# Performance work log

Hardware: AMD Instinct MI355X
Metric: run time of the kernel (lower is better)

The kernel has to match this reference:

```python
import jax, jax.numpy as jnp
import numpy as np

EPS = 1e-6
D = 512      # embedding_dim
M = 4        # n_modules
B = 4        # batch
S = 128      # seq_len
K = 32       # stack_size
STEPS = 16   # max_steps (ACT)
SCALE = D ** (-0.5)


def _clin(zr, zi, Wr, Wi, sub):
    # complex linear: (Wr + i Wi)(zr + i zi), torch Linear convention y = x @ W.T
    yr = jnp.einsum(sub, zr, Wr) - jnp.einsum(sub, zi, Wi)
    yi = jnp.einsum(sub, zi, Wr) + jnp.einsum(sub, zr, Wi)
    return yr, yi


def forward_fn(x_real, x_imag, Wl_r, Wl_i, Wq_r, Wq_i, Wk_r, Wk_i, Wv_r, Wv_i,
               ln_scale, ln_shift, mod_bias, gate_mask,
               score_w, score_b, conf_w, conf_b, halt_w, halt_b,
               ctrl_w, ctrl_b, st_score_w, st_score_b, st_conf_w, st_conf_b):
    mem0 = jnp.zeros((B, K, 2 * D), x_real.dtype)
    ptr0 = jnp.zeros((B, K), x_real.dtype).at[:, 0].set(1.0)
    acc0 = jnp.zeros((B, S, 2 * D), x_real.dtype)
    rem0 = jnp.ones((B,), x_real.dtype)

    def step(carry, _):
        sr, si, mem, ptr, acc, rem = carry
        # ComplexAttentionBlock (all M modules vectorized on axis m)
        cr = 0.5 * x_real + 0.5 * sr
        ci = 0.5 * x_imag + 0.5 * si
        zr, zi = _clin(cr, ci, Wl_r, Wl_i, 'bsd,mod->bmso')   # [B,M,S,D]
        # ComplexLayerNorm (magnitude LN, unbiased var as torch.var default)
        mag = jnp.sqrt(zr * zr + zi * zi) + EPS
        mean = mag.mean(-1, keepdims=True)
        var = mag.var(-1, keepdims=True, ddof=1)
        nm = (mag - mean) / jnp.sqrt(var + EPS)
        nm = nm * ln_scale[None, :, None, :] + ln_shift[None, :, None, :]
        ph = jnp.arctan2(zi, zr)
        zr = nm * jnp.cos(ph)
        zi = nm * jnp.sin(ph)
        # ModReLU
        nrm = jnp.sqrt(zr * zr + zi * zi) + EPS
        sc = jax.nn.relu(nrm + mod_bias[None, :, None, :]) / nrm
        zr = zr * sc
        zi = zi * sc
        # ComplexAttention over concatenated real/imag q,k
        sub = 'bmsd,mod->bmso'
        qr, qi = _clin(zr, zi, Wq_r, Wq_i, sub)
        kr, ki = _clin(zr, zi, Wk_r, Wk_i, sub)
        vr, vi = _clin(zr, zi, Wv_r, Wv_i, sub)
        qf = jnp.concatenate([qr, qi], -1)   # [B,M,S,2D]
        kf = jnp.concatenate([kr, ki], -1)
        attn = jax.nn.softmax(jnp.einsum('bmse,bmte->bmst', qf, kf) * SCALE, axis=-1)
        ar = jnp.einsum('bmst,bmtd->bmsd', attn, vr)
        ai = jnp.einsum('bmst,bmtd->bmsd', attn, vi)
        # SigmoidGatingMask
        g = jax.nn.sigmoid(gate_mask)[None, :, None, :]
        pr = ar * g
        pi = ai * g
        flat = jnp.concatenate([pr, pi], -1)  # [B,M,S,2D]
        score = jnp.einsum('bmse,me->bms', flat, score_w) + score_b[None, :, None]
        conf = jax.nn.sigmoid(jnp.einsum('bmse,me->bms', flat, conf_w) + conf_b[None, :, None])
        halt = jnp.einsum('bmse,me->bms', flat, halt_w) + halt_b[None, :, None]
        # DifferentiableStack on seq-pooled broadcast state
        flat_in = jnp.concatenate([sr.mean(1), si.mean(1)], -1)  # [B,2D]
        control = jax.nn.softmax(flat_in @ ctrl_w + ctrl_b, axis=-1)  # [B,3]
        push, pop, noop = control[:, 0:1], control[:, 1:2], control[:, 2:3]
        ptr_up = jnp.roll(ptr, 1, axis=1)
        ptr_dn = jnp.roll(ptr, -1, axis=1)
        new_ptr = push * ptr_up + pop * ptr_dn + noop * ptr
        new_ptr = new_ptr / (new_ptr.sum(1, keepdims=True) + EPS)
        wmask = push * ptr_up                                   # [B,K]
        new_mem = wmask[..., None] * flat_in[:, None, :] + mem * (1.0 - wmask[..., None])
        read = (new_mem * new_ptr[..., None]).sum(1)            # [B,2D]
        sp_r, sp_i = read[:, :D], read[:, D:]
        st_sc = read @ st_score_w + st_score_b[0]               # [B]
        st_cf = jax.nn.sigmoid(read @ st_conf_w + st_conf_b[0])
        # combine M block proposals + stack proposal via score*confidence softmax
        all_pr = jnp.concatenate([pr, jnp.broadcast_to(sp_r[:, None, None, :], (B, 1, S, D))], 1)
        all_pi = jnp.concatenate([pi, jnp.broadcast_to(sp_i[:, None, None, :], (B, 1, S, D))], 1)
        all_sc = jnp.concatenate([score, jnp.broadcast_to(st_sc[:, None, None], (B, 1, S))], 1)
        all_cf = jnp.concatenate([conf, jnp.broadcast_to(st_cf[:, None, None], (B, 1, S))], 1)
        w = jax.nn.softmax(all_sc * all_cf, axis=1)[..., None]  # [B,M+1,S,1]
        new_sr = (w * all_pr).sum(1)
        new_si = (w * all_pi).sum(1)
        # ACT halting accumulation
        p = jax.nn.sigmoid(halt).mean(axis=(1, 2))              # [B]
        acc = acc + (p * rem)[:, None, None] * jnp.concatenate([new_sr, new_si], -1)
        rem = rem * (1.0 - p)
        return (new_sr, new_si, new_mem, new_ptr, acc, rem), None

    carry, _ = jax.lax.scan(step, (x_real, x_imag, mem0, ptr0, acc0, rem0), None, length=STEPS)
    sr, si, _, _, acc, rem = carry
    # add ACT remainder weight on final state
    out = acc + rem[:, None, None] * jnp.concatenate([sr, si], -1)
    return out  # [B,S,2D] real/imag concat


def setup_inputs() -> dict:
    key = jax.random.key(0)
    ks = jax.random.split(key, 24)
    w = 1.0 / np.sqrt(D)
    h = 0.02
    inp = {
        'x_real': jax.random.normal(ks[0], (B, S, D), jnp.float32),
        'x_imag': jax.random.normal(ks[1], (B, S, D), jnp.float32),
        'Wl_r': jax.random.normal(ks[2], (M, D, D), jnp.float32) * w,
        'Wl_i': jax.random.normal(ks[3], (M, D, D), jnp.float32) * w,
        'Wq_r': jax.random.normal(ks[4], (M, D, D), jnp.float32) * w,
        'Wq_i': jax.random.normal(ks[5], (M, D, D), jnp.float32) * w,
        'Wk_r': jax.random.normal(ks[6], (M, D, D), jnp.float32) * w,
        'Wk_i': jax.random.normal(ks[7], (M, D, D), jnp.float32) * w,
        'Wv_r': jax.random.normal(ks[8], (M, D, D), jnp.float32) * w,
        'Wv_i': jax.random.normal(ks[9], (M, D, D), jnp.float32) * w,
        'ln_scale': jnp.ones((M, D), jnp.float32),
        'ln_shift': jnp.zeros((M, D), jnp.float32),
        'mod_bias': jnp.zeros((M, D), jnp.float32),
        'gate_mask': jnp.ones((M, D), jnp.float32),
        'score_w': jax.random.normal(ks[10], (M, 2 * D), jnp.float32) * h,
        'score_b': jnp.zeros((M,), jnp.float32),
        'conf_w': jax.random.normal(ks[11], (M, 2 * D), jnp.float32) * h,
        'conf_b': jnp.zeros((M,), jnp.float32),
        'halt_w': jax.random.normal(ks[12], (M, 2 * D), jnp.float32) * h,
        'halt_b': jnp.full((M,), -4.0, jnp.float32),  # nn.init.constant_(halt_head.bias, -4.0)
        'ctrl_w': jax.random.normal(ks[13], (2 * D, 3), jnp.float32) * h,
        'ctrl_b': jnp.zeros((3,), jnp.float32),
        'st_score_w': jax.random.normal(ks[14], (2 * D,), jnp.float32) * h,
        'st_score_b': jnp.zeros((1,), jnp.float32),
        'st_conf_w': jax.random.normal(ks[15], (2 * D,), jnp.float32) * h,
        'st_conf_b': jnp.zeros((1,), jnp.float32),
    }
    return inp


def reference(x_real, x_imag, Wl_r, Wl_i, Wq_r, Wq_i, Wk_r, Wk_i, Wv_r, Wv_i,
              ln_scale, ln_shift, mod_bias, gate_mask,
              score_w, score_b, conf_w, conf_b, halt_w, halt_b,
              ctrl_w, ctrl_b, st_score_w, st_score_b, st_conf_w, st_conf_b):
    return forward_fn(x_real, x_imag, Wl_r, Wl_i, Wq_r, Wq_i, Wk_r, Wk_i, Wv_r, Wv_i,
                      ln_scale, ln_shift, mod_bias, gate_mask,
                      score_w, score_b, conf_w, conf_b, halt_w, halt_b,
                      ctrl_w, ctrl_b, st_score_w, st_score_b, st_conf_w, st_conf_b)
```

## Files before the change

kernel.cpp:

```cpp
#include <hip/hip_runtime.h>

#define DD 512
#define MM 4
#define BB 4
#define SS 128
#define KK 32
#define NSTEPS 16
#define EPSF 1e-6f
#define SCALEF 0.04419417382415922f

typedef unsigned short u16;
typedef __bf16 bf16x8 __attribute__((ext_vector_type(8)));
typedef u16 u16x8 __attribute__((ext_vector_type(8)));
typedef float f32x16 __attribute__((ext_vector_type(16)));

__device__ inline void split_bf16(float x, u16& h, u16& l) {
  __bf16 hb = (__bf16)x;
  float hf = (float)hb;
  __bf16 lb = (__bf16)(x - hf);
  h = __builtin_bit_cast(u16, hb);
  l = __builtin_bit_cast(u16, lb);
}

__global__ void k_convw(const float* __restrict__ src, u16* __restrict__ dst) {
  int idx = blockIdx.x * 256 + threadIdx.x;
  int row = idx >> 9, k = idx & 511;
  u16 h, l;
  split_bf16(src[idx], h, l);
  dst[(size_t)row * 1024 + k] = h;
  dst[(size_t)row * 1024 + 512 + k] = l;
}

__global__ void k_init(const float* __restrict__ xr, const float* __restrict__ xi,
                       float* __restrict__ sr, float* __restrict__ si,
                       float* __restrict__ acc, float* __restrict__ memv,
                       float* __restrict__ ptrv, float* __restrict__ rem,
                       u16* __restrict__ crbf, u16* __restrict__ cibf) {
  int idx = blockIdx.x * 256 + threadIdx.x;
  if (idx < BB * SS * 2 * DD) acc[idx] = 0.f;
  if (idx < BB * SS * DD) {
    float a = xr[idx], b = xi[idx];
    sr[idx] = a; si[idx] = b;
    int row = idx >> 9, d = idx & 511;
    u16 h, l;
    split_bf16(a, h, l);
    crbf[(size_t)row * 1024 + d] = h;
    crbf[(size_t)row * 1024 + 512 + d] = l;
    split_bf16(b, h, l);
    cibf[(size_t)row * 1024 + d] = h;
    cibf[(size_t)row * 1024 + 512 + d] = l;
  }
  if (idx < BB * KK * 2 * DD) memv[idx] = 0.f;
  if (idx < BB * KK) ptrv[idx] = ((idx & (KK - 1)) == 0) ? 1.f : 0.f;
  if (idx < BB) rem[idx] = 1.f;
}

__global__ void k_flatctrl(const float* __restrict__ sr, const float* __restrict__ si,
                           const float* __restrict__ ctrl_w, const float* __restrict__ ctrl_b,
                           float* __restrict__ ptrv, float* __restrict__ flat_in,
                           float* __restrict__ nptrg, float* __restrict__ wmg,
                           float* __restrict__ stacc,
                           float* __restrict__ scorev, float* __restrict__ confv,
                           float* __restrict__ haltv) {
  int b = blockIdx.x;
  int tid = threadIdx.x;
  __shared__ float red[3 * 256];
  __shared__ float ctrl[3], optr[KK], nptr_s[KK], wm_s[KK], normf;

  if (tid < KK) optr[tid] = ptrv[b * KK + tid];

#pragma unroll
  for (int i = 0; i < 2; i++) {
    int r = b * MM * SS + tid + i * 256;
    scorev[r] = 0.f; confv[r] = 0.f; haltv[r] = 0.f;
  }

  int e4 = tid * 4;
  const float* basep = (e4 < DD) ? sr : si;
  int d4 = (e4 < DD) ? e4 : (e4 - DD);
  float4 accv = make_float4(0.f, 0.f, 0.f, 0.f);
  size_t base = (size_t)b * SS * DD + d4;
  for (int s = 0; s < SS; s++) {
    float4 v = *(const float4*)&basep[base + (size_t)s * DD];
    accv.x += v.x; accv.y += v.y; accv.z += v.z; accv.w += v.w;
  }
  accv.x *= (1.0f / SS); accv.y *= (1.0f / SS); accv.z *= (1.0f / SS); accv.w *= (1.0f / SS);
  *(float4*)&flat_in[b * 2 * DD + e4] = accv;
  float fv[4] = {accv.x, accv.y, accv.z, accv.w};
  float d0 = 0.f, d1 = 0.f, d2 = 0.f;
#pragma unroll
  for (int j = 0; j < 4; j++) {
    d0 += fv[j] * ctrl_w[(e4 + j) * 3 + 0];
    d1 += fv[j] * ctrl_w[(e4 + j) * 3 + 1];
    d2 += fv[j] * ctrl_w[(e4 + j) * 3 + 2];
  }
  red[tid] = d0; red[256 + tid] = d1; red[512 + tid] = d2;
  __syncthreads();
  for (int off = 128; off > 0; off >>= 1) {
    if (tid < off) {
      red[tid] += red[tid + off];
      red[256 + tid] += red[256 + tid + off];
      red[512 + tid] += red[512 + tid + off];
    }
    __syncthreads();
  }
  if (tid == 0) {
    float l0 = red[0] + ctrl_b[0], l1 = red[256] + ctrl_b[1], l2 = red[512] + ctrl_b[2];
    float mx = fmaxf(l0, fmaxf(l1, l2));
    float e0 = expf(l0 - mx), e1 = expf(l1 - mx), e2 = expf(l2 - mx);
    float s = e0 + e1 + e2;
    ctrl[0] = e0 / s; ctrl[1] = e1 / s; ctrl[2] = e2 / s;
    stacc[b * 2] = 0.f; stacc[b * 2 + 1] = 0.f;
  }
  __syncthreads();
  if (tid < KK) {
    float up = optr[(tid + KK - 1) & (KK - 1)];
    float dn = optr[(tid + 1) & (KK - 1)];
    float cu = optr[tid];
    nptr_s[tid] = ctrl[0] * up + ctrl[1] * dn + ctrl[2] * cu;
    wm_s[tid] = ctrl[0] * up;
  }
  __syncthreads();
  if (tid == 0) {
    float s = 0.f;
    for (int k = 0; k < KK; k++) s += nptr_s[k];
    normf = 1.f / (s + EPSF);
  }
  __syncthreads();
  if (tid < KK) {
    float np = nptr_s[tid] * normf;
    ptrv[b * KK + tid] = np;
    nptrg[b * KK + tid] = np;
    wmg[b * KK + tid] = wm_s[tid];
  }
}

#define LSTR 72

__global__ __launch_bounds__(256) void k_gemm_mfma(
    const u16* __restrict__ Ar, const u16* __restrict__ Ai,
    const u16* __restrict__ Wr, const u16* __restrict__ Wi,
    float* __restrict__ Cr, float* __restrict__ Ci) {
  __shared__ u16 sAr[64][LSTR], sAi[64][LSTR], sWr[64][LSTR], sWi[64][LSTR];
  int m = blockIdx.z;
  int row_blk = blockIdx.y * 64, o_blk = blockIdx.x * 64;
  int tid = threadIdx.x;

  int lrow = tid >> 3, lk8 = (tid & 7) << 3;
  size_t arow0 = (size_t)(row_blk + lrow), arow1 = arow0 + 32;
  size_t wrow0 = (size_t)m * DD + o_blk + lrow, wrow1 = wrow0 + 32;

  int wave = tid >> 6, lane = tid & 63;
  int wrow = (wave >> 1) * 32, wcol = (wave & 1) * 32;
  int l31 = lane & 31, khalf = (lane >> 5) * 8;

  f32x16 accP, accN, accI;
  for (int i = 0; i < 16; i++) { accP[i] = 0.f; accN[i] = 0.f; accI[i] = 0.f; }

  u16x8 g0 = *(const u16x8*)&Ar[arow0 * 1024 + lk8];
  u16x8 g1 = *(const u16x8*)&Ar[arow1 * 1024 + lk8];
  u16x8 g2 = *(const u16x8*)&Ai[arow0 * 1024 + lk8];
  u16x8 g3 = *(const u16x8*)&Ai[arow1 * 1024 + lk8];
  u16x8 g4 = *(const u16x8*)&Wr[wrow0 * 1024 + lk8];
  u16x8 g5 = *(const u16x8*)&Wr[wrow1 * 1024 + lk8];
  u16x8 g6 = *(const u16x8*)&Wi[wrow0 * 1024 + lk8];
  u16x8 g7 = *(const u16x8*)&Wi[wrow1 * 1024 + lk8];

  for (int it = 0; it < 24; ++it) {
    __syncthreads();
    *(u16x8*)&sAr[lrow][lk8] = g0;
    *(u16x8*)&sAr[lrow + 32][lk8] = g1;
    *(u16x8*)&sAi[lrow][lk8] = g2;
    *(u16x8*)&sAi[lrow + 32][lk8] = g3;
    *(u16x8*)&sWr[lrow][lk8] = g4;
    *(u16x8*)&sWr[lrow + 32][lk8] = g5;
    *(u16x8*)&sWi[lrow][lk8] = g6;
    *(u16x8*)&sWi[lrow + 32][lk8] = g7;
    u16x8 n0, n1, n2, n3, n4, n5, n6, n7;
    if (it < 23) {
      int it2 = it + 1, seg = it2 >> 3, k0 = (it2 & 7) * 64;
      int aofs = (seg == 1) ? 512 : 0, wofs = (seg == 2) ? 512 : 0;
      n0 = *(const u16x8*)&Ar[arow0 * 1024 + aofs + k0 + lk8];
      n1 = *(const u16x8*)&Ar[arow1 * 1024 + aofs + k0 + lk8];
      n2 = *(const u16x8*)&Ai[arow0 * 1024 + aofs + k0 + lk8];
      n3 = *(const u16x8*)&Ai[arow1 * 1024 + aofs + k0 + lk8];
      n4 = *(const u16x8*)&Wr[wrow0 * 1024 + wofs + k0 + lk8];
      n5 = *(const u16x8*)&Wr[wrow1 * 1024 + wofs + k0 + lk8];
      n6 = *(const u16x8*)&Wi[wrow0 * 1024 + wofs + k0 + lk8];
      n7 = *(const u16x8*)&Wi[wrow1 * 1024 + wofs + k0 + lk8];
    }
    __syncthreads();
#pragma unroll
    for (int kk = 0; kk < 64; kk += 16) {
      bf16x8 fAr = *(const bf16x8*)&sAr[wrow + l31][kk + khalf];
      bf16x8 fAi = *(const bf16x8*)&sAi[wrow + l31][kk + khalf];
      bf16x8 fWr = *(const bf16x8*)&sWr[wcol + l31][kk + khalf];
      bf16x8 fWi = *(const bf16x8*)&sWi[wcol + l31][kk + khalf];
      accP = __builtin_amdgcn_mfma_f32_32x32x16_bf16(fAr, fWr, accP, 0, 0, 0);
      accN = __builtin_amdgcn_mfma_f32_32x32x16_bf16(fAi, fWi, accN, 0, 0, 0);
      accI = __builtin_amdgcn_mfma_f32_32x32x16_bf16(fAi, fWr, accI, 0, 0, 0);
      accI = __builtin_amdgcn_mfma_f32_32x32x16_bf16(fAr, fWi, accI, 0, 0, 0);
    }
    if (it < 23) {
      g0 = n0; g1 = n1; g2 = n2; g3 = n3; g4 = n4; g5 = n5; g6 = n6; g7 = n7;
    }
  }

  int o = o_blk + wcol + l31;
#pragma unroll
  for (int reg = 0; reg < 16; reg++) {
    int r_in = (reg & 3) + 8 * (reg >> 2) + 4 * (lane >> 5);
    int gr = row_blk + wrow + r_in;
    int b = gr >> 7, s = gr & (SS - 1);
    size_t crow = (size_t)((b * MM + m) * SS + s);
    Cr[crow * DD + o] = accP[reg] - accN[reg];
    Ci[crow * DD + o] = accI[reg];
  }
}

__global__ __launch_bounds__(256) void k_gemm_qkv(
    const u16* __restrict__ Ar, const u16* __restrict__ Ai,
    const u16* __restrict__ wbf, size_t WSLOT,
    u16* __restrict__ qbr, u16* __restrict__ qbi,
    u16* __restrict__ kbr, u16* __restrict__ kbi,
    u16* __restrict__ vbr, u16* __restrict__ vbi) {
  __shared__ u16 sAr[64][LSTR], sAi[64][LSTR], sWr[64][LSTR], sWi[64][LSTR];
  int zid = blockIdx.z;
  int m = zid / 3, w = zid - 3 * m;
  const u16* Wr = wbf + (size_t)(2 + 2 * w) * WSLOT;
  const u16* Wi = Wr + WSLOT;
  int row_blk = blockIdx.y * 64, o_blk = blockIdx.x * 64;
  int tid = threadIdx.x;

  int lrow = tid >> 3, lk8 = (tid & 7) << 3;
  int gr0 = row_blk + lrow, gr1 = gr0 + 32;
  size_t arow0 = (size_t)(((gr0 >> 7) * MM + m) * SS + (gr0 & (SS - 1)));
  size_t arow1 = (size_t)(((gr1 >> 7) * MM + m) * SS + (gr1 & (SS - 1)));
  size_t wrow0 = (size_t)m * DD + o_blk + lrow, wrow1 = wrow0 + 32;

  int wave = tid >> 6, lane = tid & 63;
  int wrow = (wave >> 1) * 32, wcol = (wave & 1) * 32;
  int l31 = lane & 31, khalf = (lane >> 5) * 8;

  f32x16 accP, accN, accI;
  for (int i = 0; i < 16; i++) { accP[i] = 0.f; accN[i] = 0.f; accI[i] = 0.f; }

  u16x8 g0 = *(const u16x8*)&Ar[arow0 * 1024 + lk8];
  u16x8 g1 = *(const u16x8*)&Ar[arow1 * 1024 + lk8];
  u16x8 g2 = *(const u16x8*)&Ai[arow0 * 1024 + lk8];
  u16x8 g3 = *(const u16x8*)&Ai[arow1 * 1024 + lk8];
  u16x8 g4 = *(const u16x8*)&Wr[wrow0 * 1024 + lk8];
  u16x8 g5 = *(const u16x8*)&Wr[wrow1 * 1024 + lk8];
  u16x8 g6 = *(const u16x8*)&Wi[wrow0 * 1024 + lk8];
  u16x8 g7 = *(const u16x8*)&Wi[wrow1 * 1024 + lk8];

  for (int it = 0; it < 24; ++it) {
    __syncthreads();
    *(u16x8*)&sAr[lrow][lk8] = g0;
    *(u16x8*)&sAr[lrow + 32][lk8] = g1;
    *(u16x8*)&sAi[lrow][lk8] = g2;
    *(u16x8*)&sAi[lrow + 32][lk8] = g3;
    *(u16x8*)&sWr[lrow][lk8] = g4;
    *(u16x8*)&sWr[lrow + 32][lk8] = g5;
    *(u16x8*)&sWi[lrow][lk8] = g6;
    *(u16x8*)&sWi[lrow + 32][lk8] = g7;
    u16x8 n0, n1, n2, n3, n4, n5, n6, n7;
    if (it < 23) {
      int it2 = it + 1, seg = it2 >> 3, k0 = (it2 & 7) * 64;
      int aofs = (seg == 1) ? 512 : 0, wofs = (seg == 2) ? 512 : 0;
      n0 = *(const u16x8*)&Ar[arow0 * 1024 + aofs + k0 + lk8];
      n1 = *(const u16x8*)&Ar[arow1 * 1024 + aofs + k0 + lk8];
      n2 = *(const u16x8*)&Ai[arow0 * 1024 + aofs + k0 + lk8];
      n3 = *(const u16x8*)&Ai[arow1 * 1024 + aofs + k0 + lk8];
      n4 = *(const u16x8*)&Wr[wrow0 * 1024 + wofs + k0 + lk8];
      n5 = *(const u16x8*)&Wr[wrow1 * 1024 + wofs + k0 + lk8];
      n6 = *(const u16x8*)&Wi[wrow0 * 1024 + wofs + k0 + lk8];
      n7 = *(const u16x8*)&Wi[wrow1 * 1024 + wofs + k0 + lk8];
    }
    __syncthreads();
#pragma unroll
    for (int kk = 0; kk < 64; kk += 16) {
      bf16x8 fAr = *(const bf16x8*)&sAr[wrow + l31][kk + khalf];
      bf16x8 fAi = *(const bf16x8*)&sAi[wrow + l31][kk + khalf];
      bf16x8 fWr = *(const bf16x8*)&sWr[wcol + l31][kk + khalf];
      bf16x8 fWi = *(const bf16x8*)&sWi[wcol + l31][kk + khalf];
      accP = __builtin_amdgcn_mfma_f32_32x32x16_bf16(fAr, fWr, accP, 0, 0, 0);
      accN = __builtin_amdgcn_mfma_f32_32x32x16_bf16(fAi, fWi, accN, 0, 0, 0);
      accI = __builtin_amdgcn_mfma_f32_32x32x16_bf16(fAi, fWr, accI, 0, 0, 0);
      accI = __builtin_amdgcn_mfma_f32_32x32x16_bf16(fAr, fWi, accI, 0, 0, 0);
    }
    if (it < 23) {
      g0 = n0; g1 = n1; g2 = n2; g3 = n3; g4 = n4; g5 = n5; g6 = n6; g7 = n7;
    }
  }

  u16* Cr = (w == 0) ? qbr : ((w == 1) ? kbr : vbr);
  u16* Ci = (w == 0) ? qbi : ((w == 1) ? kbi : vbi);
  int o = o_blk + wcol + l31;
#pragma unroll
  for (int reg = 0; reg < 16; reg++) {
    int r_in = (reg & 3) + 8 * (reg >> 2) + 4 * (lane >> 5);
    int gr = row_blk + wrow + r_in;
    int b = gr >> 7, s = gr & (SS - 1);
    size_t crow = (size_t)((b * MM + m) * SS + s);
    u16 h, l;
    split_bf16(accP[reg] - accN[reg], h, l);
    Cr[crow * 1024 + o] = h;
    Cr[crow * 1024 + 512 + o] = l;
    split_bf16(accI[reg], h, l);
    Ci[crow * 1024 + o] = h;
    Ci[crow * 1024 + 512 + o] = l;
  }
}

__global__ __launch_bounds__(256) void k_scores_sm(
    const u16* __restrict__ Q_r, const u16* __restrict__ Q_i,
    const u16* __restrict__ K_r, const u16* __restrict__ K_i,
    u16* __restrict__ Pb) {
  __shared__ __align__(16) char smem[55296];
  u16 (*sQr)[LSTR] = (u16(*)[LSTR])smem;
  u16 (*sQi)[LSTR] = (u16(*)[LSTR])(smem + 9216);
  u16 (*sKr)[LSTR] = (u16(*)[LSTR])(smem + 18432);
  u16 (*sKi)[LSTR] = (u16(*)[LSTR])(smem + 36864);
  float (*stile)[132] = (float(*)[132])smem;

  int bm = blockIdx.z;
  int s_blk = blockIdx.y * 64;
  int tid = threadIdx.x;
  int lrow = tid >> 3, lk8 = (tid & 7) << 3;
  size_t qrow0 = (size_t)(bm * SS + s_blk + lrow), qrow1 = qrow0 + 32;
  size_t krow = (size_t)(bm * SS + lrow);

  int wave = tid >> 6, lane = tid & 63;
  int srow_w = (wave & 1) * 32;
  int tcol_w = (wave >> 1) * 64;
  int l31 = lane & 31, khalf = (lane >> 5) * 8;

  f32x16 acc0, acc1;
  for (int i = 0; i < 16; i++) { acc0[i] = 0.f; acc1[i] = 0.f; }

  for (int it = 0; it < 24; ++it) {
    int seg = it >> 3, k0 = (it & 7) * 64;
    int qofs = (seg == 1) ? 512 : 0;
    int kofs = (seg == 2) ? 512 : 0;
    u16x8 q0 = *(const u16x8*)&Q_r[qrow0 * 1024 + qofs + k0 + lk8];
    u16x8 q1 = *(const u16x8*)&Q_r[qrow1 * 1024 + qofs + k0 + lk8];
    u16x8 q2 = *(const u16x8*)&Q_i[qrow0 * 1024 + qofs + k0 + lk8];
    u16x8 q3 = *(const u16x8*)&Q_i[qrow1 * 1024 + qofs + k0 + lk8];
    u16x8 kr0 = *(const u16x8*)&K_r[(krow + 0) * 1024 + kofs + k0 + lk8];
    u16x8 kr1 = *(const u16x8*)&K_r[(krow + 32) * 1024 + kofs + k0 + lk8];
    u16x8 kr2 = *(const u16x8*)&K_r[(krow + 64) * 1024 + kofs + k0 + lk8];
    u16x8 kr3 = *(const u16x8*)&K_r[(krow + 96) * 1024 + kofs + k0 + lk8];
    u16x8 ki0 = *(const u16x8*)&K_i[(krow + 0) * 1024 + kofs + k0 + lk8];
    u16x8 ki1 = *(const u16x8*)&K_i[(krow + 32) * 1024 + kofs + k0 + lk8];
    u16x8 ki2 = *(const u16x8*)&K_i[(krow + 64) * 1024 + kofs + k0 + lk8];
    u16x8 ki3 = *(const u16x8*)&K_i[(krow + 96) * 1024 + kofs + k0 + lk8];
    __syncthreads();
    *(u16x8*)&sQr[lrow][lk8] = q0;
    *(u16x8*)&sQr[lrow + 32][lk8] = q1;
    *(u16x8*)&sQi[lrow][lk8] = q2;
    *(u16x8*)&sQi[lrow + 32][lk8] = q3;
    *(u16x8*)&sKr[lrow][lk8] = kr0;
    *(u16x8*)&sKr[lrow + 32][lk8] = kr1;
    *(u16x8*)&sKr[lrow + 64][lk8] = kr2;
    *(u16x8*)&sKr[lrow + 96][lk8] = kr3;
    *(u16x8*)&sKi[lrow][lk8] = ki0;
    *(u16x8*)&sKi[lrow + 32][lk8] = ki1;
    *(u16x8*)&sKi[lrow + 64][lk8] = ki2;
    *(u16x8*)&sKi[lrow + 96][lk8] = ki3;
    __syncthreads();
#pragma unroll
    for (int kk = 0; kk < 64; kk += 16) {
      bf16x8 fQr = *(const bf16x8*)&sQr[srow_w + l31][kk + khalf];
      bf16x8 fQi = *(const bf16x8*)&sQi[srow_w + l31][kk + khalf];
      bf16x8 fKr0 = *(const bf16x8*)&sKr[tcol_w + l31][kk + khalf];
      bf16x8 fKr1 = *(const bf16x8*)&sKr[tcol_w + 32 + l31][kk + khalf];
      bf16x8 fKi0 = *(const bf16x8*)&sKi[tcol_w + l31][kk + khalf];
      bf16x8 fKi1 = *(const bf16x8*)&sKi[tcol_w + 32 + l31][kk + khalf];
      acc0 = __builtin_amdgcn_mfma_f32_32x32x16_bf16(fQr, fKr0, acc0, 0, 0, 0);
      acc0 = __builtin_amdgcn_mfma_f32_32x32x16_bf16(fQi, fKi0, acc0, 0, 0, 0);
      acc1 = __builtin_amdgcn_mfma_f32_32x32x16_bf16(fQr, fKr1, acc1, 0, 0, 0);
      acc1 = __builtin_amdgcn_mfma_f32_32x32x16_bf16(fQi, fKi1, acc1, 0, 0, 0);
    }
  }

  __syncthreads();
#pragma unroll
  for (int reg = 0; reg < 16; reg++) {
    int r = srow_w + (reg & 3) + 8 * (reg >> 2) + 4 * (lane >> 5);
    stile[r][tcol_w + l31] = acc0[reg] * SCALEF;
    stile[r][tcol_w + 32 + l31] = acc1[reg] * SCALEF;
  }
  __syncthreads();
  int row = tid >> 2;
  int quarter = tid & 3;
  float mx = -3.4e38f;
#pragma unroll
  for (int j = 0; j < 32; j++) mx = fmaxf(mx, stile[row][quarter * 32 + j]);
  mx = fmaxf(mx, __shfl_xor(mx, 1));
  mx = fmaxf(mx, __shfl_xor(mx, 2));
  float ev[32];
  float sum = 0.f;
#pragma unroll
  for (int j = 0; j < 32; j++) {
    ev[j] = expf(stile[row][quarter * 32 + j] - mx);
    sum += ev[j];
  }
  sum += __shfl_xor(sum, 1);
  sum += __shfl_xor(sum, 2);
  float inv = 1.f / sum;
  size_t prow = (size_t)(bm * SS + s_blk + row) * 256;
#pragma unroll
  for (int j = 0; j < 32; j++) {
    int c = quarter * 32 + j;
    u16 h, l;
    split_bf16(ev[j] * inv, h, l);
    Pb[prow + c] = h;
    Pb[prow + 128 + c] = l;
  }
}

__global__ __launch_bounds__(256) void k_pv(
    const u16* __restrict__ Pb, const u16* __restrict__ vbr, const u16* __restrict__ vbi,
    const float* __restrict__ gate_mask,
    const float* __restrict__ score_w, const float* __restrict__ conf_w,
    const float* __restrict__ halt_w,
    float* __restrict__ pr, float* __restrict__ pi,
    float* __restrict__ scorev, float* __restrict__ confv, float* __restrict__ haltv) {
  __shared__ u16 sP[64][LSTR], sVr[64][LSTR], sVi[64][LSTR];
  int bm = blockIdx.z;
  int m = bm & (MM - 1);
  int s_blk = blockIdx.y * 64;
  int o_blk = blockIdx.x * 64;
  int tid = threadIdx.x;
  int lrow = tid >> 3, lk8 = (tid & 7) << 3;
  size_t prow0 = (size_t)(bm * SS + s_blk + lrow), prow1 = prow0 + 32;

  int wave = tid >> 6, lane = tid & 63;
  int wrow = (wave >> 1) * 32;
  int wcol = (wave & 1) * 32;
  int l31 = lane & 31, khalf = (lane >> 5) * 8;

  f32x16 accR, accI;
  for (int i = 0; i < 16; i++) { accR[i] = 0.f; accI[i] = 0.f; }

  for (int it = 0; it < 6; ++it) {
    int seg = it >> 1, k0 = (it & 1) * 64;
    int pofs = (seg == 1) ? 128 : 0;
    int vofs = (seg == 2) ? 512 : 0;
    u16x8 p0 = *(const u16x8*)&Pb[prow0 * 256 + pofs + k0 + lk8];
    u16x8 p1 = *(const u16x8*)&Pb[prow1 * 256 + pofs + k0 + lk8];
    size_t vrow0 = (size_t)(bm * SS + k0 + lrow), vrow1 = vrow0 + 32;
    u16x8 v0 = *(const u16x8*)&vbr[vrow0 * 1024 + vofs + o_blk + lk8];
    u16x8 v1 = *(const u16x8*)&vbr[vrow1 * 1024 + vofs + o_blk + lk8];
    u16x8 w0 = *(const u16x8*)&vbi[vrow0 * 1024 + vofs + o_blk + lk8];
    u16x8 w1 = *(const u16x8*)&vbi[vrow1 * 1024 + vofs + o_blk + lk8];
    __syncthreads();
    *(u16x8*)&sP[lrow][lk8] = p0;
    *(u16x8*)&sP[lrow + 32][lk8] = p1;
    *(u16x8*)&sVr[lrow][lk8] = v0;
    *(u16x8*)&sVr[lrow + 32][lk8] = v1;
    *(u16x8*)&sVi[lrow][lk8] = w0;
    *(u16x8*)&sVi[lrow + 32][lk8] = w1;
    __syncthreads();
#pragma unroll
    for (int kk = 0; kk < 64; kk += 16) {
      bf16x8 fP = *(const bf16x8*)&sP[wrow + l31][kk + khalf];
      u16x8 ar, ai;
#pragma unroll
      for (int j = 0; j < 8; j++) {
        ar[j] = sVr[kk + khalf + j][wcol + l31];
        ai[j] = sVi[kk + khalf + j][wcol + l31];
      }
      accR = __builtin_amdgcn_mfma_f32_32x32x16_bf16(fP, __builtin_bit_cast(bf16x8, ar), accR, 0, 0, 0);
      accI = __builtin_amdgcn_mfma_f32_32x32x16_bf16(fP, __builtin_bit_cast(bf16x8, ai), accI, 0, 0, 0);
    }
  }

  int d = o_blk + wcol + l31;
  float g = 1.f / (1.f + expf(-gate_mask[m * DD + d]));
  float swr = score_w[m * 2 * DD + d], swi = score_w[m * 2 * DD + DD + d];
  float cwr = conf_w[m * 2 * DD + d],  cwi = conf_w[m * 2 * DD + DD + d];
  float hwr = halt_w[m * 2 * DD + d],  hwi = halt_w[m * 2 * DD + DD + d];
#pragma unroll
  for (int reg = 0; reg < 16; reg++) {
    int r_in = (reg & 3) + 8 * (reg >> 2) + 4 * (lane >> 5);
    size_t crow = (size_t)(bm * SS + s_blk + wrow + r_in);
    float vR = accR[reg] * g, vI = accI[reg] * g;
    pr[crow * DD + d] = vR;
    pi[crow * DD + d] = vI;
    float ps = vR * swr + vI * swi;
    float pc = vR * cwr + vI * cwi;
    float ph = vR * hwr + vI * hwi;
#pragma unroll
    for (int off = 1; off < 32; off <<= 1) {
      ps += __shfl_xor(ps, off);
      pc += __shfl_xor(pc, off);
      ph += __shfl_xor(ph, off);
    }
    if (l31 == 0) {
      atomicAdd(&scorev[crow], ps);
      atomicAdd(&confv[crow], pc);
      atomicAdd(&haltv[crow], ph);
    }
  }
}

__global__ void k_lnphase(const float* __restrict__ zr, const float* __restrict__ zi,
                          const float* __restrict__ ln_scale, const float* __restrict__ ln_shift,
                          const float* __restrict__ mod_bias,
                          u16* __restrict__ zbr, u16* __restrict__ zbi) {
  int row = blockIdx.x;
  int m = (row >> 7) & (MM - 1);
  int tid = threadIdx.x;
  size_t base = (size_t)row * DD;
  float zrv[4], ziv[4], rv[4];
  float sum = 0.f, sumsq = 0.f;
#pragma unroll
  for (int i = 0; i < 4; i++) {
    int o = tid + i * 128;
    float a = zr[base + o], bv = zi[base + o];
    zrv[i] = a; ziv[i] = bv;
    float r = sqrtf(a * a + bv * bv);
    rv[i] = r;
    float mg = r + EPSF;
    sum += mg;
    sumsq += mg * mg;
  }
  __shared__ float rs[128], rq[128];
  rs[tid] = sum; rq[tid] = sumsq;
  __syncthreads();
  for (int off = 64; off > 0; off >>= 1) {
    if (tid < off) { rs[tid] += rs[tid + off]; rq[tid] += rq[tid + off]; }
    __syncthreads();
  }
  float mean = rs[0] * (1.0f / DD);
  float var = (rq[0] - (float)DD * mean * mean) * (1.0f / (DD - 1));
  float inv = 1.0f / sqrtf(var + EPSF);
#pragma unroll
  for (int i = 0; i < 4; i++) {
    int o = tid + i * 128;
    float mg = rv[i] + EPSF;
    float nm = (mg - mean) * inv * ln_scale[m * DD + o] + ln_shift[m * DD + o];
    float r = rv[i];
    float cosp, sinp;
    if (r > 0.f) { cosp = zrv[i] / r; sinp = ziv[i] / r; }
    else { cosp = 1.f; sinp = 0.f; }
    float z1r = nm * cosp, z1i = nm * sinp;
    float nrm = sqrtf(z1r * z1r + z1i * z1i) + EPSF;
    float sc = fmaxf(nrm + mod_bias[m * DD + o], 0.f) / nrm;
    u16 h, l;
    split_bf16(z1r * sc, h, l);
    zbr[(size_t)row * 1024 + o] = h;
    zbr[(size_t)row * 1024 + 512 + o] = l;
    split_bf16(z1i * sc, h, l);
    zbi[(size_t)row * 1024 + o] = h;
    zbi[(size_t)row * 1024 + 512 + o] = l;
  }
}

__global__ void k_memup(const float* __restrict__ flat_in,
                        const float* __restrict__ nptrg, const float* __restrict__ wmg,
                        float* __restrict__ memv, float* __restrict__ readv,
                        const float* __restrict__ st_score_w, const float* __restrict__ st_conf_w,
                        float* __restrict__ stacc) {
  int b = blockIdx.x >> 2;
  int chunk = blockIdx.x & 3;
  int tid = threadIdx.x;
  int e = chunk * 256 + tid;
  __shared__ float nptr[KK], wm[KK];
  __shared__ float red[256], red2[256];
  if (tid < KK) { nptr[tid] = nptrg[b * KK + tid]; wm[tid] = wmg[b * KK + tid]; }
  __syncthreads();
  float fl = flat_in[b * 2 * DD + e];
  float racc = 0.f;
#pragma unroll
  for (int k = 0; k < KK; k++) {
    size_t idx = ((size_t)(b * KK + k)) * 2 * DD + e;
    float nm = wm[k] * fl + memv[idx] * (1.f - wm[k]);
    memv[idx] = nm;
    racc += nm * nptr[k];
  }
  readv[b * 2 * DD + e] = racc;
  red[tid] = racc * st_score_w[e];
  red2[tid] = racc * st_conf_w[e];
  __syncthreads();
  for (int off = 128; off > 0; off >>= 1) {
    if (tid < off) { red[tid] += red[tid + off]; red2[tid] += red2[tid + off]; }
    __syncthreads();
  }
  if (tid == 0) {
    atomicAdd(&stacc[b * 2], red[0]);
    atomicAdd(&stacc[b * 2 + 1], red2[0]);
  }
}

__global__ void k_haltp(const float* __restrict__ halt, const float* __restrict__ halt_b,
                        float* __restrict__ rem,
                        float* __restrict__ coeff, const float* __restrict__ stacc,
                        const float* __restrict__ st_score_b, const float* __restrict__ st_conf_b,
                        float* __restrict__ stv) {
  int b = blockIdx.x;
  int tid = threadIdx.x;
  __shared__ float red[256];
  float v0 = halt[b * MM * SS + tid] + halt_b[tid >> 7];
  float v1 = halt[b * MM * SS + 256 + tid] + halt_b[(tid + 256) >> 7];
  red[tid] = 1.f / (1.f + expf(-v0)) + 1.f / (1.f + expf(-v1));
  __syncthreads();
  for (int off = 128; off > 0; off >>= 1) {
    if (tid < off) red[tid] += red[tid + off];
    __syncthreads();
  }
  if (tid == 0) {
    float p = red[0] * (1.0f / (MM * SS));
    float r = rem[b];
    coeff[b] = p * r;
    rem[b] = r * (1.f - p);
    stv[b] = stacc[b * 2] + st_score_b[0];
    stv[BB + b] = 1.f / (1.f + expf(-(stacc[b * 2 + 1] + st_conf_b[0])));
  }
}

__global__ void k_combine(const float* __restrict__ pr, const float* __restrict__ pi,
                          const float* __restrict__ score, const float* __restrict__ conf,
                          const float* __restrict__ score_b, const float* __restrict__ conf_b,
                          const float* __restrict__ stv, const float* __restrict__ readv,
                          const float* __restrict__ coeff,
                          const float* __restrict__ xr, const float* __restrict__ xi,
                          float* __restrict__ sr, float* __restrict__ si, float* __restrict__ acc,
                          u16* __restrict__ crbf, u16* __restrict__ cibf) {
  int bs = blockIdx.x;
  int b = bs >> 7, s = bs & (SS - 1);
  int tid = threadIdx.x;
  __shared__ float w[5];
  if (tid == 0) {
    float l[5];
    for (int m = 0; m < MM; m++) {
      int r = (b * MM + m) * SS + s;
      float sc = score[r] + score_b[m];
      float cf = 1.f / (1.f + expf(-(conf[r] + conf_b[m])));
      l[m] = sc * cf;
    }
    l[4] = stv[b] * stv[BB + b];
    float mx = l[0];
    for (int j = 1; j < 5; j++) mx = fmaxf(mx, l[j]);
    float sum = 0.f;
    for (int j = 0; j < 5; j++) { l[j] = expf(l[j] - mx); sum += l[j]; }
    for (int j = 0; j < 5; j++) w[j] = l[j] / sum;
  }
  __syncthreads();
  float cf = coeff[b];
#pragma unroll
  for (int i = 0; i < 2; i++) {
    int d = tid + i * 256;
    float nsr = w[4] * readv[b * 2 * DD + d];
    float nsi = w[4] * readv[b * 2 * DD + DD + d];
#pragma unroll
    for (int m = 0; m < MM; m++) {
      size_t off = ((size_t)((b * MM + m) * SS + s)) * DD + d;
      nsr += w[m] * pr[off];
      nsi += w[m] * pi[off];
    }
    size_t sidx = (size_t)bs * DD + d;
    sr[sidx] = nsr;
    si[sidx] = nsi;
    size_t aoff = (size_t)bs * 2 * DD;
    acc[aoff + d] += cf * nsr;
    acc[aoff + DD + d] += cf * nsi;
    u16 h, l;
    split_bf16(0.5f * xr[sidx] + 0.5f * nsr, h, l);
    crbf[(size_t)bs * 1024 + d] = h;
    crbf[(size_t)bs * 1024 + 512 + d] = l;
    split_bf16(0.5f * xi[sidx] + 0.5f * nsi, h, l);
    cibf[(size_t)bs * 1024 + d] = h;
    cibf[(size_t)bs * 1024 + 512 + d] = l;
  }
}

__global__ void k_final(const float* __restrict__ acc, const float* __restrict__ rem,
                        const float* __restrict__ sr, const float* __restrict__ si,
                        float* __restrict__ out) {
  int idx = blockIdx.x * 256 + threadIdx.x;
  int e = idx & (2 * DD - 1);
  int bs = idx >> 10;
  int b = bs >> 7;
  float v = (e < DD) ? sr[(size_t)bs * DD + e] : si[(size_t)bs * DD + e - DD];
  out[idx] = acc[idx] + rem[b] * v;
}

extern "C" void kernel_launch(void* const* d_in, const int* in_sizes, int n_in,
                              void* d_out, int out_size, void* d_ws, size_t ws_size,
                              hipStream_t stream) {
  const float* xr = (const float*)d_in[0];
  const float* xi = (const float*)d_in[1];
  const float* Wl_r = (const float*)d_in[2];
  const float* Wl_i = (const float*)d_in[3];
  const float* Wq_r = (const float*)d_in[4];
  const float* Wq_i = (const float*)d_in[5];
  const float* Wk_r = (const float*)d_in[6];
  const float* Wk_i = (const float*)d_in[7];
  const float* Wv_r = (const float*)d_in[8];
  const float* Wv_i = (const float*)d_in[9];
  const float* ln_scale = (const float*)d_in[10];
  const float* ln_shift = (const float*)d_in[11];
  const float* mod_bias = (const float*)d_in[12];
  const float* gate_mask = (const float*)d_in[13];
  const float* score_w = (const float*)d_in[14];
  const float* score_b = (const float*)d_in[15];
  const float* conf_w = (const float*)d_in[16];
  const float* conf_b = (const float*)d_in[17];
  const float* halt_w = (const float*)d_in[18];
  const float* halt_b = (const float*)d_in[19];
  const float* ctrl_w = (const float*)d_in[20];
  const float* ctrl_b = (const float*)d_in[21];
  const float* st_score_w = (const float*)d_in[22];
  const float* st_score_b = (const float*)d_in[23];
  const float* st_conf_w = (const float*)d_in[24];
  const float* st_conf_b = (const float*)d_in[25];
  float* out = (float*)d_out;

  const int BSD = BB * SS * DD;
  const int BMSD = BB * MM * SS * DD;
  const size_t WSLOT = (size_t)MM * DD * 1024;

  char* pc = (char*)d_ws;
  float* sr = (float*)pc; pc += (size_t)BSD * 4;
  float* si = (float*)pc; pc += (size_t)BSD * 4;
  float* zr = (float*)pc; pc += (size_t)BMSD * 4;
  float* zi = (float*)pc; pc += (size_t)BMSD * 4;
  float* prb = (float*)pc; pc += (size_t)BMSD * 4;
  float* pib = (float*)pc; pc += (size_t)BMSD * 4;
  float* scorev = (float*)pc; pc += (size_t)BB * MM * SS * 4;
  float* confv = (float*)pc; pc += (size_t)BB * MM * SS * 4;
  float* haltv = (float*)pc; pc += (size_t)BB * MM * SS * 4;
  float* flat = (float*)pc; pc += (size_t)BB * 2 * DD * 4;
  float* stacc = (float*)pc; pc += 64;
  float* nptrg = (float*)pc; pc += (size_t)BB * KK * 4;
  float* wmg = (float*)pc; pc += (size_t)BB * KK * 4;
  float* memv = (float*)pc; pc += (size_t)BB * KK * 2 * DD * 4;
  float* ptrv = (float*)pc; pc += (size_t)BB * KK * 4;
  float* readv = (float*)pc; pc += (size_t)BB * 2 * DD * 4;
  float* stv = (float*)pc; pc += (size_t)2 * BB * 4;
  float* accb = (float*)pc; pc += (size_t)BB * SS * 2 * DD * 4;
  float* rem = (float*)pc; pc += (size_t)BB * 4;
  float* coeff = (float*)pc; pc += (size_t)BB * 4;
  u16* crbf = (u16*)pc; pc += (size_t)BB * SS * 1024 * 2;
  u16* cibf = (u16*)pc; pc += (size_t)BB * SS * 1024 * 2;
  u16* zbr = (u16*)pc; pc += (size_t)BB * MM * SS * 1024 * 2;
  u16* zbi = (u16*)pc; pc += (size_t)BB * MM * SS * 1024 * 2;
  u16* qbr = (u16*)pc; pc += (size_t)BB * MM * SS * 1024 * 2;
  u16* qbi = (u16*)pc; pc += (size_t)BB * MM * SS * 1024 * 2;
  u16* kbr = (u16*)pc; pc += (size_t)BB * MM * SS * 1024 * 2;
  u16* kbi = (u16*)pc; pc += (size_t)BB * MM * SS * 1024 * 2;
  u16* vbr = (u16*)pc; pc += (size_t)BB * MM * SS * 1024 * 2;
  u16* vbi = (u16*)pc; pc += (size_t)BB * MM * SS * 1024 * 2;
  u16* Pb  = (u16*)pc; pc += (size_t)BB * MM * SS * 256 * 2;
  u16* wbf = (u16*)pc; pc += 8 * WSLOT * 2;

  k_convw<<<4096, 256, 0, stream>>>(Wl_r, wbf + 0 * WSLOT);
  k_convw<<<4096, 256, 0, stream>>>(Wl_i, wbf + 1 * WSLOT);
  k_convw<<<4096, 256, 0, stream>>>(Wq_r, wbf + 2 * WSLOT);
  k_convw<<<4096, 256, 0, stream>>>(Wq_i, wbf + 3 * WSLOT);
  k_convw<<<4096, 256, 0, stream>>>(Wk_r, wbf + 4 * WSLOT);
  k_convw<<<4096, 256, 0, stream>>>(Wk_i, wbf + 5 * WSLOT);
  k_convw<<<4096, 256, 0, stream>>>(Wv_r, wbf + 6 * WSLOT);
  k_convw<<<4096, 256, 0, stream>>>(Wv_i, wbf + 7 * WSLOT);

  k_init<<<2048, 256, 0, stream>>>(xr, xi, sr, si, accb, memv, ptrv, rem, crbf, cibf);

  dim3 ggrid(DD / 64, (BB * SS) / 64, MM);
  dim3 qgrid(DD / 64, (BB * SS) / 64, MM * 3);
  dim3 smgrid(1, SS / 64, BB * MM);
  dim3 pvgrid(DD / 64, SS / 64, BB * MM);

  for (int step = 0; step < NSTEPS; ++step) {
    k_flatctrl<<<BB, 256, 0, stream>>>(sr, si, ctrl_w, ctrl_b, ptrv, flat, nptrg, wmg, stacc,
                                       scorev, confv, haltv);
    k_gemm_mfma<<<ggrid, 256, 0, stream>>>(crbf, cibf, wbf + 0 * WSLOT, wbf + 1 * WSLOT, zr, zi);
    k_lnphase<<<BB * MM * SS, 128, 0, stream>>>(zr, zi, ln_scale, ln_shift, mod_bias, zbr, zbi);
    k_gemm_qkv<<<qgrid, 256, 0, stream>>>(zbr, zbi, wbf, WSLOT, qbr, qbi, kbr, kbi, vbr, vbi);
    k_scores_sm<<<smgrid, 256, 0, stream>>>(qbr, qbi, kbr, kbi, Pb);
    k_pv<<<pvgrid, 256, 0, stream>>>(Pb, vbr, vbi, gate_mask, score_w, conf_w, halt_w,
                                     prb, pib, scorev, confv, haltv);
    k_memup<<<BB * 4, 256, 0, stream>>>(flat, nptrg, wmg, memv, readv,
                                        st_score_w, st_conf_w, stacc);
    k_haltp<<<BB, 256, 0, stream>>>(haltv, halt_b, rem, coeff, stacc, st_score_b, st_conf_b, stv);
    k_combine<<<BB * SS, 256, 0, stream>>>(prb, pib, scorev, confv, score_b, conf_b,
                                           stv, readv, coeff,
                                           xr, xi, sr, si, accb, crbf, cibf);
  }

  k_final<<<(BB * SS * 2 * DD) / 256, 256, 0, stream>>>(accb, rem, sr, si, out);
}
```

Before: 2.487 ms.

## Fold Wq and Wk into a precomputed bilinear form to skip the K projection

Precomputes a complex matrix H = Wk^H·Wq per module once, before the step loop, using transposed weights and a new GEMM kernel. Each step then projects z through H instead of computing separate Q and K, and the scores kernel takes z directly as the key side. This removes one of the three QKV projections per step (grid z shrinks from MM*3 to MM*2) and the K buffers. The cost is one extra setup GEMM plus transposes, and the bf16 hi/lo rounding of the fused product H may change accuracy slightly.

New measurement: 2.273 ms. 8.6% less time.

```diff
diff --git a/kernel.cpp b/kernel.cpp
--- a/kernel.cpp
+++ b/kernel.cpp
@@ -13,6 +13,7 @@
 typedef __bf16 bf16x8 __attribute__((ext_vector_type(8)));
 typedef u16 u16x8 __attribute__((ext_vector_type(8)));
 typedef float f32x16 __attribute__((ext_vector_type(16)));
+typedef unsigned int u32x4 __attribute__((ext_vector_type(4)));
 
 __device__ inline void split_bf16(float x, u16& h, u16& l) {
   __bf16 hb = (__bf16)x;
@@ -29,6 +30,30 @@
   split_bf16(src[idx], h, l);
   dst[(size_t)row * 1024 + k] = h;
   dst[(size_t)row * 1024 + 512 + k] = l;
+}
+
+__global__ void k_convt(const float* __restrict__ src, u16* __restrict__ dst) {
+  __shared__ float tile[64][65];
+  int m = blockIdx.z;
+  int o0 = blockIdx.y * 64, d0 = blockIdx.x * 64;
+  int tid = threadIdx.x;
+  int g = tid >> 6, lane = tid & 63;
+#pragma unroll
+  for (int i = 0; i < 16; i++) {
+    int o_l = g * 16 + i;
+    tile[o_l][lane] = src[(size_t)(m * 512 + o0 + o_l) * 512 + d0 + lane];
+  }
+  __syncthreads();
+#pragma unroll
+  for (int i = 0; i < 16; i++) {
+    int d_l = g * 16 + i;
+    float v = tile[lane][d_l];
+    u16 h, l;
+    split_bf16(v, h, l);
+    size_t drow = (size_t)(m * 512 + d0 + d_l) * 1024;
+    dst[drow + o0 + lane] = h;
+    dst[drow + 512 + o0 + lane] = l;
+  }
 }
 
 __global__ void k_init(const float* __restrict__ xr, const float* __restrict__ xi,
@@ -218,25 +243,18 @@
   }
 }
 
-__global__ __launch_bounds__(256) void k_gemm_qkv(
+__global__ __launch_bounds__(256) void k_gemm_g(
     const u16* __restrict__ Ar, const u16* __restrict__ Ai,
-    const u16* __restrict__ wbf, size_t WSLOT,
-    u16* __restrict__ qbr, u16* __restrict__ qbi,
-    u16* __restrict__ kbr, u16* __restrict__ kbi,
-    u16* __restrict__ vbr, u16* __restrict__ vbi) {
+    const u16* __restrict__ Wr, const u16* __restrict__ Wi,
+    float* __restrict__ Hr, float* __restrict__ Hi) {
   __shared__ u16 sAr[64][LSTR], sAi[64][LSTR], sWr[64][LSTR], sWi[64][LSTR];
-  int zid = blockIdx.z;
-  int m = zid / 3, w = zid - 3 * m;
-  const u16* Wr = wbf + (size_t)(2 + 2 * w) * WSLOT;
-  const u16* Wi = Wr + WSLOT;
+  int m = blockIdx.z;
   int row_blk = blockIdx.y * 64, o_blk = blockIdx.x * 64;
   int tid = threadIdx.x;
 
   int lrow = tid >> 3, lk8 = (tid & 7) << 3;
-  int gr0 = row_blk + lrow, gr1 = gr0 + 32;
-  size_t arow0 = (size_t)(((gr0 >> 7) * MM + m) * SS + (gr0 & (SS - 1)));
-  size_t arow1 = (size_t)(((gr1 >> 7) * MM + m) * SS + (gr1 & (SS - 1)));
-  size_t wrow0 = (size_t)m * DD + o_blk + lrow, wrow1 = wrow0 + 32;
+  size_t arow0 = (size_t)(m * 512 + row_blk + lrow), arow1 = arow0 + 32;
+  size_t wrow0 = (size_t)(m * 512 + o_blk + lrow), wrow1 = wrow0 + 32;
 
   int wave = tid >> 6, lane = tid & 63;
   int wrow = (wave >> 1) * 32, wcol = (wave & 1) * 32;
@@ -284,6 +302,95 @@
       bf16x8 fAi = *(const bf16x8*)&sAi[wrow + l31][kk + khalf];
       bf16x8 fWr = *(const bf16x8*)&sWr[wcol + l31][kk + khalf];
       bf16x8 fWi = *(const bf16x8*)&sWi[wcol + l31][kk + khalf];
+      u32x4 t = __builtin_bit_cast(u32x4, fAi) ^ 0x80008000u;
+      bf16x8 nAi = __builtin_bit_cast(bf16x8, t);
+      accP = __builtin_amdgcn_mfma_f32_32x32x16_bf16(fAr, fWr, accP, 0, 0, 0);
+      accN = __builtin_amdgcn_mfma_f32_32x32x16_bf16(fAi, fWi, accN, 0, 0, 0);
+      accI = __builtin_amdgcn_mfma_f32_32x32x16_bf16(fAr, fWi, accI, 0, 0, 0);
+      accI = __builtin_amdgcn_mfma_f32_32x32x16_bf16(nAi, fWr, accI, 0, 0, 0);
+    }
+    if (it < 23) {
+      g0 = n0; g1 = n1; g2 = n2; g3 = n3; g4 = n4; g5 = n5; g6 = n6; g7 = n7;
+    }
+  }
+
+  int o = o_blk + wcol + l31;
+#pragma unroll
+  for (int reg = 0; reg < 16; reg++) {
+    int r_in = (reg & 3) + 8 * (reg >> 2) + 4 * (lane >> 5);
+    int gr = row_blk + wrow + r_in;
+    size_t crow = (size_t)(m * 512 + gr);
+    Hr[crow * DD + o] = accP[reg] + accN[reg];
+    Hi[crow * DD + o] = accI[reg];
+  }
+}
+
+__global__ __launch_bounds__(256) void k_gemm_qkv(
+    const u16* __restrict__ Ar, const u16* __restrict__ Ai,
+    const u16* __restrict__ wbf, size_t WSLOT,
+    u16* __restrict__ qbr, u16* __restrict__ qbi,
+    u16* __restrict__ vbr, u16* __restrict__ vbi) {
+  __shared__ u16 sAr[64][LSTR], sAi[64][LSTR], sWr[64][LSTR], sWi[64][LSTR];
+  int zid = blockIdx.z;
+  int m = zid >> 1, w = zid & 1;
+  int slot = (w == 0) ? 8 : 6;
+  const u16* Wr = wbf + (size_t)slot * WSLOT;
+  const u16* Wi = Wr + WSLOT;
+  int row_blk = blockIdx.y * 64, o_blk = blockIdx.x * 64;
+  int tid = threadIdx.x;
+
+  int lrow = tid >> 3, lk8 = (tid & 7) << 3;
+  int gr0 = row_blk + lrow, gr1 = gr0 + 32;
+  size_t arow0 = (size_t)(((gr0 >> 7) * MM + m) * SS + (gr0 & (SS - 1)));
+  size_t arow1 = (size_t)(((gr1 >> 7) * MM + m) * SS + (gr1 & (SS - 1)));
+  size_t wrow0 = (size_t)m * DD + o_blk + lrow, wrow1 = wrow0 + 32;
+
+  int wave = tid >> 6, lane = tid & 63;
+  int wrow = (wave >> 1) * 32, wcol = (wave & 1) * 32;
+  int l31 = lane & 31, khalf = (lane >> 5) * 8;
+
+  f32x16 accP, accN, accI;
+  for (int i = 0; i < 16; i++) { accP[i] = 0.f; accN[i] = 0.f; accI[i] = 0.f; }
+
+  u16x8 g0 = *(const u16x8*)&Ar[arow0 * 1024 + lk8];
+  u16x8 g1 = *(const u16x8*)&Ar[arow1 * 1024 + lk8];
+  u16x8 g2 = *(const u16x8*)&Ai[arow0 * 1024 + lk8];
+  u16x8 g3 = *(const u16x8*)&Ai[arow1 * 1024 + lk8];
+  u16x8 g4 = *(const u16x8*)&Wr[wrow0 * 1024 + lk8];
+  u16x8 g5 = *(const u16x8*)&Wr[wrow1 * 1024 + lk8];
+  u16x8 g6 = *(const u16x8*)&Wi[wrow0 * 1024 + lk8];
+  u16x8 g7 = *(const u16x8*)&Wi[wrow1 * 1024 + lk8];
+
+  for (int it = 0; it < 24; ++it) {
+    __syncthreads();
+    *(u16x8*)&sAr[lrow][lk8] = g0;
+    *(u16x8*)&sAr[lrow + 32][lk8] = g1;
+    *(u16x8*)&sAi[lrow][lk8] = g2;
+    *(u16x8*)&sAi[lrow + 32][lk8] = g3;
+    *(u16x8*)&sWr[lrow][lk8] = g4;
+    *(u16x8*)&sWr[lrow + 32][lk8] = g5;
+    *(u16x8*)&sWi[lrow][lk8] = g6;
+    *(u16x8*)&sWi[lrow + 32][lk8] = g7;
+    u16x8 n0, n1, n2, n3, n4, n5, n6, n7;
+    if (it < 23) {
+      int it2 = it + 1, seg = it2 >> 3, k0 = (it2 & 7) * 64;
+      int aofs = (seg == 1) ? 512 : 0, wofs = (seg == 2) ? 512 : 0;
+      n0 = *(const u16x8*)&Ar[arow0 * 1024 + aofs + k0 + lk8];
+      n1 = *(const u16x8*)&Ar[arow1 * 1024 + aofs + k0 + lk8];
+      n2 = *(const u16x8*)&Ai[arow0 * 1024 + aofs + k0 + lk8];
+      n3 = *(const u16x8*)&Ai[arow1 * 1024 + aofs + k0 + lk8];
+      n4 = *(const u16x8*)&Wr[wrow0 * 1024 + wofs + k0 + lk8];
+      n5 = *(const u16x8*)&Wr[wrow1 * 1024 + wofs + k0 + lk8];
+      n6 = *(const u16x8*)&Wi[wrow0 * 1024 + wofs + k0 + lk8];
+      n7 = *(const u16x8*)&Wi[wrow1 * 1024 + wofs + k0 + lk8];
+    }
+    __syncthreads();
+#pragma unroll
+    for (int kk = 0; kk < 64; kk += 16) {
+      bf16x8 fAr = *(const bf16x8*)&sAr[wrow + l31][kk + khalf];
+      bf16x8 fAi = *(const bf16x8*)&sAi[wrow + l31][kk + khalf];
+      bf16x8 fWr = *(const bf16x8*)&sWr[wcol + l31][kk + khalf];
+      bf16x8 fWi = *(const bf16x8*)&sWi[wcol + l31][kk + khalf];
       accP = __builtin_amdgcn_mfma_f32_32x32x16_bf16(fAr, fWr, accP, 0, 0, 0);
       accN = __builtin_amdgcn_mfma_f32_32x32x16_bf16(fAi, fWi, accN, 0, 0, 0);
       accI = __builtin_amdgcn_mfma_f32_32x32x16_bf16(fAi, fWr, accI, 0, 0, 0);
@@ -294,8 +401,8 @@
     }
   }
 
-  u16* Cr = (w == 0) ? qbr : ((w == 1) ? kbr : vbr);
-  u16* Ci = (w == 0) ? qbi : ((w == 1) ? kbi : vbi);
+  u16* Cr = (w == 0) ? qbr : vbr;
+  u16* Ci = (w == 0) ? qbi : vbi;
   int o = o_blk + wcol + l31;
 #pragma unroll
   for (int reg = 0; reg < 16; reg++) {
@@ -750,26 +857,37 @@
   u16* zbi = (u16*)pc; pc += (size_t)BB * MM * SS * 1024 * 2;
   u16* qbr = (u16*)pc; pc += (size_t)BB * MM * SS * 1024 * 2;
   u16* qbi = (u16*)pc; pc += (size_t)BB * MM * SS * 1024 * 2;
-  u16* kbr = (u16*)pc; pc += (size_t)BB * MM * SS * 1024 * 2;
-  u16* kbi = (u16*)pc; pc += (size_t)BB * MM * SS * 1024 * 2;
   u16* vbr = (u16*)pc; pc += (size_t)BB * MM * SS * 1024 * 2;
   u16* vbi = (u16*)pc; pc += (size_t)BB * MM * SS * 1024 * 2;
   u16* Pb  = (u16*)pc; pc += (size_t)BB * MM * SS * 256 * 2;
-  u16* wbf = (u16*)pc; pc += 8 * WSLOT * 2;
+  u16* wbf = (u16*)pc; pc += 10 * WSLOT * 2;
+  u16* wqtr = (u16*)pc; pc += WSLOT * 2;
+  u16* wqti = (u16*)pc; pc += WSLOT * 2;
+  u16* wktr = (u16*)pc; pc += WSLOT * 2;
+  u16* wkti = (u16*)pc; pc += WSLOT * 2;
+  float* hfr = (float*)pc; pc += (size_t)MM * DD * DD * 4;
+  float* hfi = (float*)pc; pc += (size_t)MM * DD * DD * 4;
 
   k_convw<<<4096, 256, 0, stream>>>(Wl_r, wbf + 0 * WSLOT);
   k_convw<<<4096, 256, 0, stream>>>(Wl_i, wbf + 1 * WSLOT);
-  k_convw<<<4096, 256, 0, stream>>>(Wq_r, wbf + 2 * WSLOT);
-  k_convw<<<4096, 256, 0, stream>>>(Wq_i, wbf + 3 * WSLOT);
-  k_convw<<<4096, 256, 0, stream>>>(Wk_r, wbf + 4 * WSLOT);
-  k_convw<<<4096, 256, 0, stream>>>(Wk_i, wbf + 5 * WSLOT);
   k_convw<<<4096, 256, 0, stream>>>(Wv_r, wbf + 6 * WSLOT);
   k_convw<<<4096, 256, 0, stream>>>(Wv_i, wbf + 7 * WSLOT);
 
+  dim3 tgrid(8, 8, 4);
+  k_convt<<<tgrid, 256, 0, stream>>>(Wq_r, wqtr);
+  k_convt<<<tgrid, 256, 0, stream>>>(Wq_i, wqti);
+  k_convt<<<tgrid, 256, 0, stream>>>(Wk_r, wktr);
+  k_convt<<<tgrid, 256, 0, stream>>>(Wk_i, wkti);
+
+  dim3 hgrid(8, 8, 4);
+  k_gemm_g<<<hgrid, 256, 0, stream>>>(wktr, wkti, wqtr, wqti, hfr, hfi);
+  k_convw<<<4096, 256, 0, stream>>>(hfr, wbf + 8 * WSLOT);
+  k_convw<<<4096, 256, 0, stream>>>(hfi, wbf + 9 * WSLOT);
+
   k_init<<<2048, 256, 0, stream>>>(xr, xi, sr, si, accb, memv, ptrv, rem, crbf, cibf);
 
   dim3 ggrid(DD / 64, (BB * SS) / 64, MM);
-  dim3 qgrid(DD / 64, (BB * SS) / 64, MM * 3);
+  dim3 qgrid(DD / 64, (BB * SS) / 64, MM * 2);
   dim3 smgrid(1, SS / 64, BB * MM);
   dim3 pvgrid(DD / 64, SS / 64, BB * MM);
 
@@ -778,8 +896,8 @@
                                        scorev, confv, haltv);
     k_gemm_mfma<<<ggrid, 256, 0, stream>>>(crbf, cibf, wbf + 0 * WSLOT, wbf + 1 * WSLOT, zr, zi);
     k_lnphase<<<BB * MM * SS, 128, 0, stream>>>(zr, zi, ln_scale, ln_shift, mod_bias, zbr, zbi);
-    k_gemm_qkv<<<qgrid, 256, 0, stream>>>(zbr, zbi, wbf, WSLOT, qbr, qbi, kbr, kbi, vbr, vbi);
-    k_scores_sm<<<smgrid, 256, 0, stream>>>(qbr, qbi, kbr, kbi, Pb);
+    k_gemm_qkv<<<qgrid, 256, 0, stream>>>(zbr, zbi, wbf, WSLOT, qbr, qbi, vbr, vbi);
+    k_scores_sm<<<smgrid, 256, 0, stream>>>(qbr, qbi, zbr, zbi, Pb);
     k_pv<<<pvgrid, 256, 0, stream>>>(Pb, vbr, vbi, gate_mask, score_w, conf_w, halt_w,
                                      prb, pib, scorev, confv, haltv);
     k_memup<<<BB * 4, 256, 0, stream>>>(flat, nptrg, wmg, memv, readv,
```
